# Optimization experiments

Hardware: AMD Instinct MI355X
Metric: run time of the kernel (lower is better)

The kernel has to match this reference:

```python
import jax, jax.numpy as jnp
import numpy as np

B, S, I, H = 64, 1024, 256, 256

def setup_inputs() -> dict:
    key = jax.random.key(0)
    k1, k2, k3 = jax.random.split(key, 3)
    x = jax.random.normal(k1, (B, S, I), dtype=jnp.float32)
    W = jax.random.normal(k2, (4 * H, H + I), dtype=jnp.float32) * (1.0 / np.sqrt(H + I))
    b = jax.random.normal(k3, (4 * H,), dtype=jnp.float32) * 0.01
    return {"x": x, "W": W, "b": b}

def reference(x, W, b):
    batch, seq_len, input_size = x.shape
    hidden = W.shape[1] - input_size
    # torch concat order is (hidden, x): first H columns of W act on h, rest on x
    W_h = W[:, :hidden]          # [4H, H]
    W_x = W[:, hidden:]          # [4H, I]
    # precompute input projections for all timesteps: [B, S, 4H]
    x_proj = jnp.einsum('bsi,gi->bsg', x, W_x) + b

    h0 = jnp.zeros((batch, hidden), dtype=x.dtype)
    c0 = jnp.zeros((batch, hidden), dtype=x.dtype)

    def step(carry, xp_t):
        h, c = carry
        gates = h @ W_h.T + xp_t                     # [B, 4H]
        f, i, g, o = jnp.split(gates, 4, axis=1)     # chunk order: forget, input, convert, output
        f = jax.nn.sigmoid(f)
        i = jax.nn.sigmoid(i)
        g = jnp.tanh(g)
        o = jax.nn.sigmoid(o)
        c_new = f * c + i * g
        h_new = o * jnp.tanh(c_new)
        return (h_new, c_new), h_new

    (h_fin, c_fin), outs = jax.lax.scan(step, (h0, c0), jnp.swapaxes(x_proj, 0, 1))
    outputs = jnp.swapaxes(outs, 0, 1)               # [B, S, H]
    return outputs, (h_fin, c_fin)
```

## Files before the change

kernel.cpp:

```cpp
#include <hip/hip_runtime.h>

typedef __attribute__((ext_vector_type(8))) short short8;
typedef __attribute__((ext_vector_type(4))) float f32x4;
typedef __attribute__((ext_vector_type(4))) unsigned u32x4;

__device__ __forceinline__ unsigned short f2bf(float f) {
  unsigned int u = __float_as_uint(f);
  u = (u + 0x7fffu + ((u >> 16) & 1u)) >> 16;
  return (unsigned short)u;
}

__device__ __forceinline__ void xp_store(float* p, float v) { *p = v; }
__device__ __forceinline__ void xp_store(unsigned short* p, float v) { *p = f2bf(v); }
__device__ __forceinline__ float xp_ld(const float* p) { return *p; }
__device__ __forceinline__ float xp_ld(const unsigned short* p) {
  return __uint_as_float(((unsigned int)*p) << 16);
}

__device__ __forceinline__ float quad_sum(float a) {
  float t1 = __int_as_float(
      __builtin_amdgcn_update_dpp(0, __float_as_int(a), 177, 0xf, 0xf, true));
  a += t1;
  float t2 = __int_as_float(
      __builtin_amdgcn_update_dpp(0, __float_as_int(a), 78, 0xf, 0xf, true));
  return a + t2;
}

__global__ void prep_wx(const float* __restrict__ W, unsigned int* __restrict__ Wx2) {
  int i = blockIdx.x * 256 + threadIdx.x;
  int g = i >> 7, kk = i & 127;
  float lo = W[(size_t)g * 512 + 256 + 2 * kk];
  float hi = W[(size_t)g * 512 + 256 + 2 * kk + 1];
  Wx2[i] = (unsigned int)f2bf(lo) | ((unsigned int)f2bf(hi) << 16);
}

__global__ void prep_wh(const float* __restrict__ W, unsigned int* __restrict__ Wh2) {
  int i = blockIdx.x * 256 + threadIdx.x;
  int r = i >> 7, kk = i & 127;
  float lo = W[(size_t)r * 512 + 2 * kk];
  float hi = W[(size_t)r * 512 + 2 * kk + 1];
  Wh2[i] = (unsigned int)f2bf(lo) | ((unsigned int)f2bf(hi) << 16);
}

template <typename XPT>
__global__ __launch_bounds__(256, 4) void gemm_xp(const float* __restrict__ x,
                                                  const unsigned int* __restrict__ Wx2,
                                                  const float* __restrict__ bias,
                                                  XPT* __restrict__ xp) {
  __shared__ unsigned short As[128][40];
  __shared__ unsigned short Bs[128][40];
  const int m0 = blockIdx.y * 128, n0 = blockIdx.x * 128;
  const int tid = threadIdx.x, lane = tid & 63, w = tid >> 6;
  const int wr = w >> 1, wc = w & 1;
  const int r16 = lane & 15, kq = lane >> 4;
  f32x4 acc[4][4];
#pragma unroll
  for (int m = 0; m < 4; m++)
#pragma unroll
    for (int n = 0; n < 4; n++)
#pragma unroll
      for (int j = 0; j < 4; j++) acc[m][n][j] = 0.f;

  for (int kb = 0; kb < 256; kb += 32) {
    __syncthreads();
#pragma unroll
    for (int i = 0; i < 4; i++) {
      int idx = tid + i * 256;
      int row = idx >> 3, c4 = idx & 7;
      float4 v = *(const float4*)(x + (size_t)(m0 + row) * 256 + kb + c4 * 4);
      ushort4 s;
      s.x = f2bf(v.x); s.y = f2bf(v.y); s.z = f2bf(v.z); s.w = f2bf(v.w);
      *(ushort4*)&As[row][c4 * 4] = s;
    }
#pragma unroll
    for (int i = 0; i < 2; i++) {
      int idx = tid + i * 256;
      int row = idx >> 2, c = idx & 3;
      uint4 v = *(const uint4*)(Wx2 + (size_t)(n0 + row) * 128 + (kb >> 1) + c * 4);
      *(uint4*)&Bs[row][c * 8] = v;
    }
    __syncthreads();
    short8 a[4], bb[4];
#pragma unroll
    for (int m = 0; m < 4; m++)
      a[m] = *(const short8*)&As[wr * 64 + m * 16 + r16][kq * 8];
#pragma unroll
    for (int n = 0; n < 4; n++)
      bb[n] = *(const short8*)&Bs[wc * 64 + n * 16 + r16][kq * 8];
#pragma unroll
    for (int m = 0; m < 4; m++)
#pragma unroll
      for (int n = 0; n < 4; n++)
        acc[m][n] = __builtin_amdgcn_mfma_f32_16x16x32_bf16(a[m], bb[n], acc[m][n], 0, 0, 0);
  }
#pragma unroll
  for (int n = 0; n < 4; n++) {
    int gn = n0 + wc * 64 + n * 16 + r16;
    float bi = bias[gn];
#pragma unroll
    for (int m = 0; m < 4; m++) {
      int gm = m0 + wr * 64 + m * 16 + kq * 4;
#pragma unroll
      for (int j = 0; j < 4; j++) {
        xp_store(&xp[(size_t)(gm + j) * 1024 + gn], acc[m][n][j] + bi);
      }
    }
  }
}

template <typename XPT>
__global__ __attribute__((amdgpu_flat_work_group_size(1024, 1024),
                          amdgpu_waves_per_eu(4, 4)))
void lstm_rec(const unsigned* __restrict__ Wh2,
              const XPT* __restrict__ xp,
              float* __restrict__ out) {
  __shared__ u32x4 wot[9 * 1024];
  __shared__ unsigned hsh[2][4][136];

  const int tid = threadIdx.x;
  const int b = blockIdx.x;
  const int u = tid >> 2, p = tid & 3;
  const int brow0 = b << 10;

  const unsigned* wf_p = Wh2 + (size_t)(0 * 256 + u) * 128 + (p << 5);
  const unsigned* wi_p = Wh2 + (size_t)(1 * 256 + u) * 128 + (p << 5);
  const unsigned* wg_p = Wh2 + (size_t)(2 * 256 + u) * 128 + (p << 5);
  const unsigned* wo_p = Wh2 + (size_t)(3 * 256 + u) * 128 + (p << 5);
  u32x4 wf0, wf1, wf2, wf3, wf4, wf5, wf6, wf7;
  u32x4 wi0, wi1, wi2, wi3, wi4, wi5, wi6, wi7;
  u32x4 wg0, wg1, wg2, wg3, wg4, wg5, wg6;
#define LOADROW8(P, R0, R1, R2, R3, R4, R5, R6, R7)                   \
  asm volatile("global_load_dwordx4 %0, %8, off\n\t"                  \
               "global_load_dwordx4 %1, %8, off offset:16\n\t"        \
               "global_load_dwordx4 %2, %8, off offset:32\n\t"        \
               "global_load_dwordx4 %3, %8, off offset:48\n\t"        \
               "global_load_dwordx4 %4, %8, off offset:64\n\t"        \
               "global_load_dwordx4 %5, %8, off offset:80\n\t"        \
               "global_load_dwordx4 %6, %8, off offset:96\n\t"        \
               "global_load_dwordx4 %7, %8, off offset:112"           \
               : "=&v"(R0), "=&v"(R1), "=&v"(R2), "=&v"(R3),          \
                 "=&v"(R4), "=&v"(R5), "=&v"(R6), "=&v"(R7)           \
               : "v"(P)                                               \
               : "memory")
#define LOADROW7(P, R0, R1, R2, R3, R4, R5, R6)                       \
  asm volatile("global_load_dwordx4 %0, %7, off\n\t"                  \
               "global_load_dwordx4 %1, %7, off offset:16\n\t"        \
               "global_load_dwordx4 %2, %7, off offset:32\n\t"        \
               "global_load_dwordx4 %3, %7, off offset:48\n\t"        \
               "global_load_dwordx4 %4, %7, off offset:64\n\t"        \
               "global_load_dwordx4 %5, %7, off offset:80\n\t"        \
               "global_load_dwordx4 %6, %7, off offset:96"            \
               : "=&v"(R0), "=&v"(R1), "=&v"(R2), "=&v"(R3),          \
                 "=&v"(R4), "=&v"(R5), "=&v"(R6)                      \
               : "v"(P)                                               \
               : "memory")
  LOADROW8(wf_p, wf0, wf1, wf2, wf3, wf4, wf5, wf6, wf7);
  LOADROW8(wi_p, wi0, wi1, wi2, wi3, wi4, wi5, wi6, wi7);
  LOADROW7(wg_p, wg0, wg1, wg2, wg3, wg4, wg5, wg6);
#undef LOADROW8
#undef LOADROW7
  asm volatile("s_waitcnt vmcnt(0)" ::: "memory");

#pragma unroll
  for (int E = 0; E < 8; E++) wot[(E << 10) + tid] = *(const u32x4*)(wo_p + (E << 2));
  wot[(8 << 10) + tid] = *(const u32x4*)(wg_p + 28);

  for (int i = tid; i < 2 * 4 * 136; i += 1024) ((unsigned*)hsh)[i] = 0u;
  float c = 0.f;
  float* outp = out + ((size_t)brow0 << 8);
  __syncthreads();

#define BAR() asm volatile("s_waitcnt lgkmcnt(0)\n\ts_barrier" ::: "memory")
#define DOT2(ACC, WD, HD) \
  asm("v_dot2_f32_bf16 %0, %1, %2, %0" : "+v"(ACC) : "v"(WD), "v"(HD))
#define DOTC(WF, WI, WGQ, OJ, HJ)                                   \
  {                                                                 \
    DOT2(a0, WF[0], (HJ)[0]); DOT2(a0, WF[1], (HJ)[1]);             \
    DOT2(a0, WF[2], (HJ)[2]); DOT2(a0, WF[3], (HJ)[3]);             \
    DOT2(a1, WI[0], (HJ)[0]); DOT2(a1, WI[1], (HJ)[1]);             \
    DOT2(a1, WI[2], (HJ)[2]); DOT2(a1, WI[3], (HJ)[3]);             \
    DOT2(a2, (WGQ)[0], (HJ)[0]); DOT2(a2, (WGQ)[1], (HJ)[1]);       \
    DOT2(a2, (WGQ)[2], (HJ)[2]); DOT2(a2, (WGQ)[3], (HJ)[3]);       \
    DOT2(a3, (OJ)[0], (HJ)[0]); DOT2(a3, (OJ)[1], (HJ)[1]);         \
    DOT2(a3, (OJ)[2], (HJ)[2]); DOT2(a3, (OJ)[3], (HJ)[3]);         \
  }
#define HJC(HRX, J) (*(const u32x4*)&hsh[HRX][p][(p << 5) + ((J) << 2)])

#define STEP(T, HR, HW)                                                                \
  {                                                                                    \
    const int t = (T);                                                                 \
          \
    const XPT* xr = xp + ((size_t)(brow0 + t) << 10);                                  \
    float xv0 = xp_ld(xr + u);                                                         \
    float xv1 = xp_ld(xr + 256 + u);                                                   \
    float xv2 = xp_ld(xr + 512 + u);                                                   \
    float xv3 = xp_ld(xr + 768 + u);                                                   \
                         \
    u32x4 gt7 = wot[(8 << 10) + tid];                                                  \
    u32x4 ojA = wot[(0 << 10) + tid];                                                  \
    u32x4 hjA = HJC(HR, 0);                                                            \
    u32x4 ojB = wot[(1 << 10) + tid];                                                  \
    u32x4 hjB = HJC(HR, 1);                                                            \
    float a0 = 0.f, a1 = 0.f, a2 = 0.f, a3 = 0.f;                                      \
    DOTC(wf0, wi0, wg0, ojA, hjA) ojA = wot[(2 << 10) + tid]; hjA = HJC(HR, 2);        \
    DOTC(wf1, wi1, wg1, ojB, hjB) ojB = wot[(3 << 10) + tid]; hjB = HJC(HR, 3);        \
    DOTC(wf2, wi2, wg2, ojA, hjA) ojA = wot[(4 << 10) + tid]; hjA = HJC(HR, 4);        \
    DOTC(wf3, wi3, wg3, ojB, hjB) ojB = wot[(5 << 10) + tid]; hjB = HJC(HR, 5);        \
    DOTC(wf4, wi4, wg4, ojA, hjA) ojA = wot[(6 << 10) + tid]; hjA = HJC(HR, 6);        \
    DOTC(wf5, wi5, wg5, ojB, hjB) ojB = wot[(7 << 10) + tid]; hjB = HJC(HR, 7);        \
    DOTC(wf6, wi6, wg6, ojA, hjA)                                                      \
    DOTC(wf7, wi7, gt7, ojB, hjB)                                                      \
                 \
    a0 = quad_sum(a0); a1 = quad_sum(a1); a2 = quad_sum(a2); a3 = quad_sum(a3);        \
    float gf = a0 + xv0, gi = a1 + xv1, gg = a2 + xv2, go = a3 + xv3;                  \
    float f = 1.f / (1.f + __expf(-gf));                                               \
    float ii = 1.f / (1.f + __expf(-gi));                                              \
    float eg = __expf(2.f * gg);                                                       \
    float gtv = (eg - 1.f) / (eg + 1.f);                                               \
    float o = 1.f / (1.f + __expf(-go));                                               \
    c = f * c + ii * gtv;                                                              \
    float ec = __expf(2.f * c);                                                        \
    float tc = (ec - 1.f) / (ec + 1.f);                                                \
    float h = o * tc;                                                                  \
                    \
    ((unsigned short*)&hsh[HW][p][0])[u] = f2bf(h);                                    \
    if (p == 0) {                                                                      \
      __builtin_nontemporal_store(h, outp + ((size_t)t << 8) + u);                     \
      if (t == 1023) {                                                                 \
        out[16777216 + b * 256 + u] = h;                                               \
        out[16777216 + 16384 + b * 256 + u] = c;                                       \
      }                                                                                \
    }                                                                                  \
           \
    BAR();                                                                             \
  }

  for (int t2 = 0; t2 < 1024; t2 += 2) {
    STEP(t2, 1, 0)
    STEP(t2 + 1, 0, 1)
  }
#undef STEP
#undef HJC
#undef DOTC
#undef DOT2
#undef BAR
}

extern "C" void kernel_launch(void* const* d_in, const int* in_sizes, int n_in,
                              void* d_out, int out_size, void* d_ws, size_t ws_size,
                              hipStream_t stream) {
  (void)in_sizes; (void)n_in; (void)out_size;
  const float* x = (const float*)d_in[0];
  const float* W = (const float*)d_in[1];
  const float* bias = (const float*)d_in[2];
  float* out = (float*)d_out;
  char* ws = (char*)d_ws;

  unsigned int* Wx2 = (unsigned int*)ws;
  unsigned int* Wh2 = (unsigned int*)(ws + 524288);
  char* xpmem = ws + 1048576;

  const size_t need32 = 1048576 + (size_t)65536 * 1024 * 4;

  prep_wx<<<512, 256, 0, stream>>>(W, Wx2);
  prep_wh<<<512, 256, 0, stream>>>(W, Wh2);

  if (ws_size >= need32) {
    gemm_xp<float><<<dim3(8, 512), 256, 0, stream>>>(x, Wx2, bias, (float*)xpmem);
    lstm_rec<float><<<64, 1024, 0, stream>>>(Wh2, (const float*)xpmem, out);
  } else {
    gemm_xp<unsigned short><<<dim3(8, 512), 256, 0, stream>>>(x, Wx2, bias,
                                                              (unsigned short*)xpmem);
    lstm_rec<unsigned short><<<64, 1024, 0, stream>>>(Wh2, (const unsigned short*)xpmem, out);
  }
}
```

Measured before the change: 2.303 ms.

## Halve recurrent block to 512 threads, each computing two hidden units

The recurrent LSTM kernel now launches 512 threads per batch instead of 1024. Each thread handles two hidden units (v and v+128), keeping 48 weight vectors in registers and moving all output-gate weights into LDS. The goal is a cheaper per-step barrier, amortised h loads and more independent work per thread for latency hiding. In exchange, occupancy drops to 2 waves per EU, register pressure rises sharply (risking spills), and per-thread serial work per timestep doubles.

Measured after the change: 2.106 ms (median of 3 runs). 8.6% less time.

```diff
diff --git a/kernel.cpp b/kernel.cpp
--- a/kernel.cpp
+++ b/kernel.cpp
@@ -109,26 +109,33 @@
 }
 
 template <typename XPT>
-__global__ __attribute__((amdgpu_flat_work_group_size(1024, 1024),
-                          amdgpu_waves_per_eu(4, 4)))
+__global__ __attribute__((amdgpu_flat_work_group_size(512, 512),
+                          amdgpu_waves_per_eu(2, 2)))
 void lstm_rec(const unsigned* __restrict__ Wh2,
               const XPT* __restrict__ xp,
               float* __restrict__ out) {
-  __shared__ u32x4 wot[9 * 1024];
+  __shared__ u32x4 wot[16 * 512];
   __shared__ unsigned hsh[2][4][136];
 
   const int tid = threadIdx.x;
   const int b = blockIdx.x;
-  const int u = tid >> 2, p = tid & 3;
+  const int v = tid >> 2, p = tid & 3;
   const int brow0 = b << 10;
 
-  const unsigned* wf_p = Wh2 + (size_t)(0 * 256 + u) * 128 + (p << 5);
-  const unsigned* wi_p = Wh2 + (size_t)(1 * 256 + u) * 128 + (p << 5);
-  const unsigned* wg_p = Wh2 + (size_t)(2 * 256 + u) * 128 + (p << 5);
-  const unsigned* wo_p = Wh2 + (size_t)(3 * 256 + u) * 128 + (p << 5);
-  u32x4 wf0, wf1, wf2, wf3, wf4, wf5, wf6, wf7;
-  u32x4 wi0, wi1, wi2, wi3, wi4, wi5, wi6, wi7;
-  u32x4 wg0, wg1, wg2, wg3, wg4, wg5, wg6;
+  const unsigned* fA_p = Wh2 + (size_t)(v) * 128 + (p << 5);
+  const unsigned* iA_p = Wh2 + (size_t)(256 + v) * 128 + (p << 5);
+  const unsigned* gA_p = Wh2 + (size_t)(512 + v) * 128 + (p << 5);
+  const unsigned* oA_p = Wh2 + (size_t)(768 + v) * 128 + (p << 5);
+  const unsigned* fB_p = Wh2 + (size_t)(128 + v) * 128 + (p << 5);
+  const unsigned* iB_p = Wh2 + (size_t)(384 + v) * 128 + (p << 5);
+  const unsigned* gB_p = Wh2 + (size_t)(640 + v) * 128 + (p << 5);
+  const unsigned* oB_p = Wh2 + (size_t)(896 + v) * 128 + (p << 5);
+  u32x4 fA0, fA1, fA2, fA3, fA4, fA5, fA6, fA7;
+  u32x4 iA0, iA1, iA2, iA3, iA4, iA5, iA6, iA7;
+  u32x4 gA0, gA1, gA2, gA3, gA4, gA5, gA6, gA7;
+  u32x4 fB0, fB1, fB2, fB3, fB4, fB5, fB6, fB7;
+  u32x4 iB0, iB1, iB2, iB3, iB4, iB5, iB6, iB7;
+  u32x4 gB0, gB1, gB2, gB3, gB4, gB5, gB6, gB7;
 #define LOADROW8(P, R0, R1, R2, R3, R4, R5, R6, R7)                   \
   asm volatile("global_load_dwordx4 %0, %8, off\n\t"                  \
                "global_load_dwordx4 %1, %8, off offset:16\n\t"        \
@@ -142,93 +149,109 @@
                  "=&v"(R4), "=&v"(R5), "=&v"(R6), "=&v"(R7)           \
                : "v"(P)                                               \
                : "memory")
-#define LOADROW7(P, R0, R1, R2, R3, R4, R5, R6)                       \
-  asm volatile("global_load_dwordx4 %0, %7, off\n\t"                  \
-               "global_load_dwordx4 %1, %7, off offset:16\n\t"        \
-               "global_load_dwordx4 %2, %7, off offset:32\n\t"        \
-               "global_load_dwordx4 %3, %7, off offset:48\n\t"        \
-               "global_load_dwordx4 %4, %7, off offset:64\n\t"        \
-               "global_load_dwordx4 %5, %7, off offset:80\n\t"        \
-               "global_load_dwordx4 %6, %7, off offset:96"            \
-               : "=&v"(R0), "=&v"(R1), "=&v"(R2), "=&v"(R3),          \
-                 "=&v"(R4), "=&v"(R5), "=&v"(R6)                      \
-               : "v"(P)                                               \
-               : "memory")
-  LOADROW8(wf_p, wf0, wf1, wf2, wf3, wf4, wf5, wf6, wf7);
-  LOADROW8(wi_p, wi0, wi1, wi2, wi3, wi4, wi5, wi6, wi7);
-  LOADROW7(wg_p, wg0, wg1, wg2, wg3, wg4, wg5, wg6);
+  LOADROW8(fA_p, fA0, fA1, fA2, fA3, fA4, fA5, fA6, fA7);
+  LOADROW8(iA_p, iA0, iA1, iA2, iA3, iA4, iA5, iA6, iA7);
+  LOADROW8(gA_p, gA0, gA1, gA2, gA3, gA4, gA5, gA6, gA7);
+  LOADROW8(fB_p, fB0, fB1, fB2, fB3, fB4, fB5, fB6, fB7);
+  LOADROW8(iB_p, iB0, iB1, iB2, iB3, iB4, iB5, iB6, iB7);
+  LOADROW8(gB_p, gB0, gB1, gB2, gB3, gB4, gB5, gB6, gB7);
 #undef LOADROW8
-#undef LOADROW7
   asm volatile("s_waitcnt vmcnt(0)" ::: "memory");
 
 #pragma unroll
-  for (int E = 0; E < 8; E++) wot[(E << 10) + tid] = *(const u32x4*)(wo_p + (E << 2));
-  wot[(8 << 10) + tid] = *(const u32x4*)(wg_p + 28);
-
-  for (int i = tid; i < 2 * 4 * 136; i += 1024) ((unsigned*)hsh)[i] = 0u;
-  float c = 0.f;
+  for (int E = 0; E < 8; E++) {
+    wot[(E << 9) + tid] = *(const u32x4*)(oA_p + (E << 2));
+    wot[((E + 8) << 9) + tid] = *(const u32x4*)(oB_p + (E << 2));
+  }
+
+  for (int i = tid; i < 2 * 4 * 136; i += 512) ((unsigned*)hsh)[i] = 0u;
+  float c0 = 0.f, c1 = 0.f;
   float* outp = out + ((size_t)brow0 << 8);
   __syncthreads();
 
 #define BAR() asm volatile("s_waitcnt lgkmcnt(0)\n\ts_barrier" ::: "memory")
 #define DOT2(ACC, WD, HD) \
   asm("v_dot2_f32_bf16 %0, %1, %2, %0" : "+v"(ACC) : "v"(WD), "v"(HD))
-#define DOTC(WF, WI, WGQ, OJ, HJ)                                   \
+#define DOTC(FA, IA, GA, FB, IB, GB, OA, OB, HJ)                    \
   {                                                                 \
-    DOT2(a0, WF[0], (HJ)[0]); DOT2(a0, WF[1], (HJ)[1]);             \
-    DOT2(a0, WF[2], (HJ)[2]); DOT2(a0, WF[3], (HJ)[3]);             \
-    DOT2(a1, WI[0], (HJ)[0]); DOT2(a1, WI[1], (HJ)[1]);             \
-    DOT2(a1, WI[2], (HJ)[2]); DOT2(a1, WI[3], (HJ)[3]);             \
-    DOT2(a2, (WGQ)[0], (HJ)[0]); DOT2(a2, (WGQ)[1], (HJ)[1]);       \
-    DOT2(a2, (WGQ)[2], (HJ)[2]); DOT2(a2, (WGQ)[3], (HJ)[3]);       \
-    DOT2(a3, (OJ)[0], (HJ)[0]); DOT2(a3, (OJ)[1], (HJ)[1]);         \
-    DOT2(a3, (OJ)[2], (HJ)[2]); DOT2(a3, (OJ)[3], (HJ)[3]);         \
+    DOT2(aF0, FA[0], (HJ)[0]); DOT2(aF0, FA[1], (HJ)[1]);           \
+    DOT2(aF0, FA[2], (HJ)[2]); DOT2(aF0, FA[3], (HJ)[3]);           \
+    DOT2(aI0, IA[0], (HJ)[0]); DOT2(aI0, IA[1], (HJ)[1]);           \
+    DOT2(aI0, IA[2], (HJ)[2]); DOT2(aI0, IA[3], (HJ)[3]);           \
+    DOT2(aG0, GA[0], (HJ)[0]); DOT2(aG0, GA[1], (HJ)[1]);           \
+    DOT2(aG0, GA[2], (HJ)[2]); DOT2(aG0, GA[3], (HJ)[3]);           \
+    DOT2(aO0, (OA)[0], (HJ)[0]); DOT2(aO0, (OA)[1], (HJ)[1]);       \
+    DOT2(aO0, (OA)[2], (HJ)[2]); DOT2(aO0, (OA)[3], (HJ)[3]);       \
+    DOT2(aF1, FB[0], (HJ)[0]); DOT2(aF1, FB[1], (HJ)[1]);           \
+    DOT2(aF1, FB[2], (HJ)[2]); DOT2(aF1, FB[3], (HJ)[3]);           \
+    DOT2(aI1, IB[0], (HJ)[0]); DOT2(aI1, IB[1], (HJ)[1]);           \
+    DOT2(aI1, IB[2], (HJ)[2]); DOT2(aI1, IB[3], (HJ)[3]);           \
+    DOT2(aG1, GB[0], (HJ)[0]); DOT2(aG1, GB[1], (HJ)[1]);           \
+    DOT2(aG1, GB[2], (HJ)[2]); DOT2(aG1, GB[3], (HJ)[3]);           \
+    DOT2(aO1, (OB)[0], (HJ)[0]); DOT2(aO1, (OB)[1], (HJ)[1]);       \
+    DOT2(aO1, (OB)[2], (HJ)[2]); DOT2(aO1, (OB)[3], (HJ)[3]);       \
   }
 #define HJC(HRX, J) (*(const u32x4*)&hsh[HRX][p][(p << 5) + ((J) << 2)])
+
+#define LSTM1(AF, AI, AG, AO, X0, X1, X2, X3, CC, HOUT)             \
+  {                                                                 \
+    float gf = AF + X0, gi = AI + X1, gg = AG + X2, go = AO + X3;   \
+    float f = 1.f / (1.f + __expf(-gf));                            \
+    float ii = 1.f / (1.f + __expf(-gi));                           \
+    float eg = __expf(2.f * gg);                                    \
+    float gtv = (eg - 1.f) / (eg + 1.f);                            \
+    float o = 1.f / (1.f + __expf(-go));                            \
+    CC = f * CC + ii * gtv;                                         \
+    float ec = __expf(2.f * CC);                                    \
+    float tc = (ec - 1.f) / (ec + 1.f);                             \
+    HOUT = o * tc;                                                  \
+  }
 
 #define STEP(T, HR, HW)                                                                \
   {                                                                                    \
     const int t = (T);                                                                 \
           \
     const XPT* xr = xp + ((size_t)(brow0 + t) << 10);                                  \
-    float xv0 = xp_ld(xr + u);                                                         \
-    float xv1 = xp_ld(xr + 256 + u);                                                   \
-    float xv2 = xp_ld(xr + 512 + u);                                                   \
-    float xv3 = xp_ld(xr + 768 + u);                                                   \
-                         \
-    u32x4 gt7 = wot[(8 << 10) + tid];                                                  \
-    u32x4 ojA = wot[(0 << 10) + tid];                                                  \
-    u32x4 hjA = HJC(HR, 0);                                                            \
-    u32x4 ojB = wot[(1 << 10) + tid];                                                  \
-    u32x4 hjB = HJC(HR, 1);                                                            \
-    float a0 = 0.f, a1 = 0.f, a2 = 0.f, a3 = 0.f;                                      \
-    DOTC(wf0, wi0, wg0, ojA, hjA) ojA = wot[(2 << 10) + tid]; hjA = HJC(HR, 2);        \
-    DOTC(wf1, wi1, wg1, ojB, hjB) ojB = wot[(3 << 10) + tid]; hjB = HJC(HR, 3);        \
-    DOTC(wf2, wi2, wg2, ojA, hjA) ojA = wot[(4 << 10) + tid]; hjA = HJC(HR, 4);        \
-    DOTC(wf3, wi3, wg3, ojB, hjB) ojB = wot[(5 << 10) + tid]; hjB = HJC(HR, 5);        \
-    DOTC(wf4, wi4, wg4, ojA, hjA) ojA = wot[(6 << 10) + tid]; hjA = HJC(HR, 6);        \
-    DOTC(wf5, wi5, wg5, ojB, hjB) ojB = wot[(7 << 10) + tid]; hjB = HJC(HR, 7);        \
-    DOTC(wf6, wi6, wg6, ojA, hjA)                                                      \
-    DOTC(wf7, wi7, gt7, ojB, hjB)                                                      \
+    float xv0 = xp_ld(xr + v),        xv1 = xp_ld(xr + 256 + v);                       \
+    float xv2 = xp_ld(xr + 512 + v),  xv3 = xp_ld(xr + 768 + v);                       \
+    float xw0 = xp_ld(xr + 128 + v),  xw1 = xp_ld(xr + 384 + v);                       \
+    float xw2 = xp_ld(xr + 640 + v),  xw3 = xp_ld(xr + 896 + v);                       \
+                                                     \
+    u32x4 hX = HJC(HR, 0), oAX = wot[(0 << 9) + tid], oBX = wot[(8 << 9) + tid];       \
+    u32x4 hY = HJC(HR, 1), oAY = wot[(1 << 9) + tid], oBY = wot[(9 << 9) + tid];       \
+    float aF0 = 0.f, aI0 = 0.f, aG0 = 0.f, aO0 = 0.f;                                  \
+    float aF1 = 0.f, aI1 = 0.f, aG1 = 0.f, aO1 = 0.f;                                  \
+    DOTC(fA0, iA0, gA0, fB0, iB0, gB0, oAX, oBX, hX)                                   \
+    hX = HJC(HR, 2); oAX = wot[(2 << 9) + tid]; oBX = wot[(10 << 9) + tid];            \
+    DOTC(fA1, iA1, gA1, fB1, iB1, gB1, oAY, oBY, hY)                                   \
+    hY = HJC(HR, 3); oAY = wot[(3 << 9) + tid]; oBY = wot[(11 << 9) + tid];            \
+    DOTC(fA2, iA2, gA2, fB2, iB2, gB2, oAX, oBX, hX)                                   \
+    hX = HJC(HR, 4); oAX = wot[(4 << 9) + tid]; oBX = wot[(12 << 9) + tid];            \
+    DOTC(fA3, iA3, gA3, fB3, iB3, gB3, oAY, oBY, hY)                                   \
+    hY = HJC(HR, 5); oAY = wot[(5 << 9) + tid]; oBY = wot[(13 << 9) + tid];            \
+    DOTC(fA4, iA4, gA4, fB4, iB4, gB4, oAX, oBX, hX)                                   \
+    hX = HJC(HR, 6); oAX = wot[(6 << 9) + tid]; oBX = wot[(14 << 9) + tid];            \
+    DOTC(fA5, iA5, gA5, fB5, iB5, gB5, oAY, oBY, hY)                                   \
+    hY = HJC(HR, 7); oAY = wot[(7 << 9) + tid]; oBY = wot[(15 << 9) + tid];            \
+    DOTC(fA6, iA6, gA6, fB6, iB6, gB6, oAX, oBX, hX)                                   \
+    DOTC(fA7, iA7, gA7, fB7, iB7, gB7, oAY, oBY, hY)                                   \
                  \
-    a0 = quad_sum(a0); a1 = quad_sum(a1); a2 = quad_sum(a2); a3 = quad_sum(a3);        \
-    float gf = a0 + xv0, gi = a1 + xv1, gg = a2 + xv2, go = a3 + xv3;                  \
-    float f = 1.f / (1.f + __expf(-gf));                                               \
-    float ii = 1.f / (1.f + __expf(-gi));                                              \
-    float eg = __expf(2.f * gg);                                                       \
-    float gtv = (eg - 1.f) / (eg + 1.f);                                               \
-    float o = 1.f / (1.f + __expf(-go));                                               \
-    c = f * c + ii * gtv;                                                              \
-    float ec = __expf(2.f * c);                                                        \
-    float tc = (ec - 1.f) / (ec + 1.f);                                                \
-    float h = o * tc;                                                                  \
-                    \
-    ((unsigned short*)&hsh[HW][p][0])[u] = f2bf(h);                                    \
+    aF0 = quad_sum(aF0); aI0 = quad_sum(aI0); aG0 = quad_sum(aG0); aO0 = quad_sum(aO0);\
+    aF1 = quad_sum(aF1); aI1 = quad_sum(aI1); aG1 = quad_sum(aG1); aO1 = quad_sum(aO1);\
+    float h0v, h1v;                                                                    \
+    LSTM1(aF0, aI0, aG0, aO0, xv0, xv1, xv2, xv3, c0, h0v)                             \
+    LSTM1(aF1, aI1, aG1, aO1, xw0, xw1, xw2, xw3, c1, h1v)                             \
+                   \
+    ((unsigned short*)&hsh[HW][p][0])[v] = f2bf(h0v);                                  \
+    ((unsigned short*)&hsh[HW][p][0])[v + 128] = f2bf(h1v);                            \
     if (p == 0) {                                                                      \
-      __builtin_nontemporal_store(h, outp + ((size_t)t << 8) + u);                     \
+      __builtin_nontemporal_store(h0v, outp + ((size_t)t << 8) + v);                   \
+      __builtin_nontemporal_store(h1v, outp + ((size_t)t << 8) + v + 128);             \
       if (t == 1023) {                                                                 \
-        out[16777216 + b * 256 + u] = h;                                               \
-        out[16777216 + 16384 + b * 256 + u] = c;                                       \
+        out[16777216 + b * 256 + v] = h0v;                                             \
+        out[16777216 + b * 256 + v + 128] = h1v;                                       \
+        out[16777216 + 16384 + b * 256 + v] = c0;                                      \
+        out[16777216 + 16384 + b * 256 + v + 128] = c1;                                \
       }                                                                                \
     }                                                                                  \
            \
@@ -240,6 +263,7 @@
     STEP(t2 + 1, 0, 1)
   }
 #undef STEP
+#undef LSTM1
 #undef HJC
 #undef DOTC
 #undef DOT2
@@ -267,10 +291,10 @@
 
   if (ws_size >= need32) {
     gemm_xp<float><<<dim3(8, 512), 256, 0, stream>>>(x, Wx2, bias, (float*)xpmem);
-    lstm_rec<float><<<64, 1024, 0, stream>>>(Wh2, (const float*)xpmem, out);
+    lstm_rec<float><<<64, 512, 0, stream>>>(Wh2, (const float*)xpmem, out);
   } else {
     gemm_xp<unsigned short><<<dim3(8, 512), 256, 0, stream>>>(x, Wx2, bias,
                                                               (unsigned short*)xpmem);
-    lstm_rec<unsigned short><<<64, 1024, 0, stream>>>(Wh2, (const unsigned short*)xpmem, out);
-  }
-}
+    lstm_rec<unsigned short><<<64, 512, 0, stream>>>(Wh2, (const unsigned short*)xpmem, out);
+  }
+}
```
